# Kernel optimization log

Hardware: AMD Instinct MI355X
Metric: run time of the kernel (lower is better)

The kernel has to match this reference:

```python
import jax, jax.numpy as jnp
import numpy as np

NI = 50000      # input nodes
NO = 50000      # output nodes
DEG = 16        # uniform neighborhood size -> E = NO*DEG
E = NO * DEG
FI = 64         # input feature dim
UNITS = 64
D = 3           # coord feature dim


def setup_inputs() -> dict:
    key = jax.random.key(0)
    k1, k2, k3, k4 = jax.random.split(key, 4)
    node_features = jax.random.normal(k1, (NI, FI), dtype=jnp.float32)
    coord_features = jax.random.normal(k2, (E, D), dtype=jnp.float32)
    indices = jax.random.randint(k3, (E,), 0, NI, dtype=jnp.int64)
    # uniform ragged structure: each output node has DEG edges
    row_splits = (jnp.arange(NO + 1, dtype=jnp.int64) * DEG)
    W = jax.random.normal(k4, (FI, UNITS * D), dtype=jnp.float32) * (1.0 / np.sqrt(FI))
    b = jnp.zeros((UNITS * D,), dtype=jnp.float32)
    return {"node_features": node_features, "coord_features": coord_features,
            "indices": indices, "row_splits": row_splits, "W": W, "b": b}


def reference(node_features, coord_features, indices, row_splits, W, b):
    # Dense projection on input nodes: [Ni, units*D]
    h = node_features @ W + b
    # gather_first=False path of ragged_convolution_transpose: gather after dense
    g = h[indices]                       # [E, units*D]
    g = g.reshape(-1, UNITS, D)          # [E, units, D]
    # contract over coord dim: f_eu = sum_d g_eud * coord_ed
    f = jnp.einsum('eud,ed->eu', g, coord_features)  # [E, units]
    # activation is None (identity)
    # ragged segment-sum via row_splits -> segment ids per edge
    num_out = row_splits.shape[0] - 1
    row_lengths = jnp.diff(row_splits)
    seg_ids = jnp.repeat(jnp.arange(num_out), row_lengths,
                         total_repeat_length=f.shape[0])
    out = jax.ops.segment_sum(f, seg_ids, num_segments=num_out)  # [No, units]
    return out
```

## Files before the change

### kernel.cpp

```cpp
#include <hip/hip_runtime.h>


#define NI 50000
#define NO 50000
#define DEG 16
#define FI 64
#define UNITS 64
#define KK 192
#define TN 16
#define SG 196
#define NBLK 1024
#define NTILES (NO / TN)

__global__ __launch_bounds__(256, 4)
void rct_fused2(const float* __restrict__ nf,
                const float* __restrict__ coord,
                const int* __restrict__ idx,
                const float* __restrict__ W,
                const float* __restrict__ b,
                float* __restrict__ out) {
    __shared__ float G[TN * SG];
    __shared__ float Pbuf[4][TN][UNITS];
    __shared__ float Cs[2][TN][4];
    __shared__ float bs[KK];

    const int tid  = threadIdx.x;
    const int w    = tid >> 6;
    const int lane = tid & 63;

    if (tid < KK) bs[tid] = b[tid];

    float wreg[48];
    #pragma unroll
    for (int j = 0; j < 48; ++j) {
        const int il = j / 3, d = j - il * 3;
        wreg[j] = W[(w * 16 + il) * KK + 3 * lane + d];
    }

    for (int t = blockIdx.x; t < NTILES; t += NBLK) {
        const int node0 = t * TN;
        const int par = t & 1;

        #pragma unroll
        for (int r = 0; r < 4; ++r) {
            const int n  = w * 4 + r;
            const int eb = (node0 + n) * DEG;
            float a0 = 0.f, a1 = 0.f, a2 = 0.f;
            float c0s = 0.f, c1s = 0.f, c2s = 0.f;
            #pragma unroll
            for (int j = 0; j < DEG; ++j) {
                const int e  = __builtin_amdgcn_readfirstlane(eb + j);
                const int id = __builtin_amdgcn_readfirstlane(idx[e]);
                const float c0 = coord[e * 3 + 0];
                const float c1 = coord[e * 3 + 1];
                const float c2 = coord[e * 3 + 2];
                const float v  = nf[id * FI + lane];
                a0 += v * c0; a1 += v * c1; a2 += v * c2;
                c0s += c0; c1s += c1; c2s += c2;
            }
            G[n * SG + 3 * lane + 0] = a0;
            G[n * SG + 3 * lane + 1] = a1;
            G[n * SG + 3 * lane + 2] = a2;
            if (lane == 0) {
                Cs[par][n][0] = c0s; Cs[par][n][1] = c1s; Cs[par][n][2] = c2s;
            }
        }
        __syncthreads();

        {
            float acc[TN];
            #pragma unroll
            for (int n = 0; n < TN; ++n) acc[n] = 0.f;
            const int kbase = w * 48;
            #pragma unroll
            for (int n = 0; n < TN; ++n) {
                const float* g = &G[n * SG + kbase];
                #pragma unroll
                for (int kk = 0; kk < 48; kk += 4) {
                    const float4 gv = *(const float4*)(g + kk);
                    acc[n] += gv.x * wreg[kk]     + gv.y * wreg[kk + 1]
                            + gv.z * wreg[kk + 2] + gv.w * wreg[kk + 3];
                }
            }
            #pragma unroll
            for (int n = 0; n < TN; ++n) Pbuf[w][n][lane] = acc[n];
        }
        __syncthreads();

        #pragma unroll
        for (int jj = 0; jj < 4; ++jj) {
            const int n = w + 4 * jj;
            const float s = Pbuf[0][n][lane] + Pbuf[1][n][lane]
                          + Pbuf[2][n][lane] + Pbuf[3][n][lane]
                          + Cs[par][n][0] * bs[3 * lane + 0]
                          + Cs[par][n][1] * bs[3 * lane + 1]
                          + Cs[par][n][2] * bs[3 * lane + 2];
            out[(node0 + n) * UNITS + lane] = s;
        }
    }
}

extern "C" void kernel_launch(void* const* d_in, const int* in_sizes, int n_in,
                              void* d_out, int out_size, void* d_ws, size_t ws_size,
                              hipStream_t stream) {
    const float* nf    = (const float*)d_in[0];
    const float* coord = (const float*)d_in[1];
    const int*   idx   = (const int*)d_in[2];
    const float* W     = (const float*)d_in[4];
    const float* b     = (const float*)d_in[5];
    float* out = (float*)d_out;

    rct_fused2<<<dim3(NBLK), dim3(256), 0, stream>>>(nf, coord, idx, W, b, out);
}
```

Before: 122.0 us.

## Replace scalar FP32 projection with split-bf16 MFMA and double-buffered LDS

The per-tile 16x192x64 projection now runs on MFMA 16x16x32 bf16 instructions instead of scalar FMAs with a cross-wave reduction. Each operand is split into high and low bf16 parts and three MFMAs are issued per step to approximate FP32 accuracy. The staged G tile is double-buffered, which removes the Pbuf reduction and the second barrier. The cost is extra bit-splitting work and some precision loss compared with true FP32. The gather phase is likely memory-bound, so the gain may be limited.

```diff
diff --git a/kernel.cpp b/kernel.cpp
--- a/kernel.cpp
+++ b/kernel.cpp
@@ -1,101 +1,105 @@
 #include <hip/hip_runtime.h>
 
 
-#define NI 50000
 #define NO 50000
 #define DEG 16
 #define FI 64
 #define UNITS 64
 #define KK 192
 #define TN 16
-#define SG 196
+#define NSTEP 6
+#define GPAD 200
 #define NBLK 1024
 #define NTILES (NO / TN)
 
+typedef __attribute__((ext_vector_type(8))) short short8;
+typedef __attribute__((ext_vector_type(4))) float float4v;
+
+static __device__ __forceinline__ unsigned int asu(float x){ union{float f;unsigned int u;}c; c.f=x; return c.u; }
+static __device__ __forceinline__ float asf(unsigned int x){ union{unsigned int u;float f;}c; c.u=x; return c.f; }
+
 __global__ __launch_bounds__(256, 4)
-void rct_fused2(const float* __restrict__ nf,
-                const float* __restrict__ coord,
-                const int* __restrict__ idx,
-                const float* __restrict__ W,
-                const float* __restrict__ b,
-                float* __restrict__ out) {
-    __shared__ float G[TN * SG];
-    __shared__ float Pbuf[4][TN][UNITS];
+void rct3(const float* __restrict__ nf, const float* __restrict__ coord,
+          const int* __restrict__ idx, const float* __restrict__ W,
+          const float* __restrict__ b, float* __restrict__ out)
+{
+    __shared__ __align__(16) unsigned short Ghi[2][TN][GPAD];
+    __shared__ __align__(16) unsigned short Glo[2][TN][GPAD];
     __shared__ float Cs[2][TN][4];
-    __shared__ float bs[KK];
 
     const int tid  = threadIdx.x;
     const int w    = tid >> 6;
     const int lane = tid & 63;
+    const int m16  = lane & 15;
+    const int quad = lane >> 4;
 
-    if (tid < KK) bs[tid] = b[tid];
+    const int u = 16 * w + m16;
+    short8 Bhi[NSTEP], Blo[NSTEP];
+    #pragma unroll
+    for (int s = 0; s < NSTEP; ++s) {
+        #pragma unroll
+        for (int j = 0; j < 8; ++j) {
+            const int k = s * 32 + quad * 8 + j;
+            const int i = k / 3, d = k - 3 * i;
+            const float v = W[i * KK + 3 * u + d];
+            const unsigned int vb = asu(v);
+            const unsigned int rh = (vb + 0x7FFFu + ((vb >> 16) & 1u)) >> 16;
+            const float hf = asf(rh << 16);
+            Bhi[s][j] = (short)rh;
+            Blo[s][j] = (short)(asu(v - hf) >> 16);
+        }
+    }
+    const float b0 = b[3*u+0], b1 = b[3*u+1], b2 = b[3*u+2];
 
-    float wreg[48];
-    #pragma unroll
-    for (int j = 0; j < 48; ++j) {
-        const int il = j / 3, d = j - il * 3;
-        wreg[j] = W[(w * 16 + il) * KK + 3 * lane + d];
-    }
-
-    for (int t = blockIdx.x; t < NTILES; t += NBLK) {
+    int pp = 0;
+    for (int t = blockIdx.x; t < NTILES; t += NBLK, pp ^= 1) {
         const int node0 = t * TN;
-        const int par = t & 1;
 
         #pragma unroll
         for (int r = 0; r < 4; ++r) {
-            const int n  = w * 4 + r;
+            const int n  = 4 * w + r;
             const int eb = (node0 + n) * DEG;
-            float a0 = 0.f, a1 = 0.f, a2 = 0.f;
-            float c0s = 0.f, c1s = 0.f, c2s = 0.f;
+            float a0=0.f,a1=0.f,a2=0.f,c0s=0.f,c1s=0.f,c2s=0.f;
             #pragma unroll
             for (int j = 0; j < DEG; ++j) {
                 const int e  = __builtin_amdgcn_readfirstlane(eb + j);
                 const int id = __builtin_amdgcn_readfirstlane(idx[e]);
-                const float c0 = coord[e * 3 + 0];
-                const float c1 = coord[e * 3 + 1];
-                const float c2 = coord[e * 3 + 2];
+                const float c0 = coord[3*e+0];
+                const float c1 = coord[3*e+1];
+                const float c2 = coord[3*e+2];
                 const float v  = nf[id * FI + lane];
-                a0 += v * c0; a1 += v * c1; a2 += v * c2;
+                a0 += v*c0; a1 += v*c1; a2 += v*c2;
                 c0s += c0; c1s += c1; c2s += c2;
             }
-            G[n * SG + 3 * lane + 0] = a0;
-            G[n * SG + 3 * lane + 1] = a1;
-            G[n * SG + 3 * lane + 2] = a2;
+            const unsigned int x0=asu(a0), x1=asu(a1), x2=asu(a2);
+            Ghi[pp][n][3*lane+0] = (unsigned short)(x0>>16);
+            Ghi[pp][n][3*lane+1] = (unsigned short)(x1>>16);
+            Ghi[pp][n][3*lane+2] = (unsigned short)(x2>>16);
+            Glo[pp][n][3*lane+0] = (unsigned short)(asu(a0 - asf(x0 & 0xFFFF0000u))>>16);
+            Glo[pp][n][3*lane+1] = (unsigned short)(asu(a1 - asf(x1 & 0xFFFF0000u))>>16);
+            Glo[pp][n][3*lane+2] = (unsigned short)(asu(a2 - asf(x2 & 0xFFFF0000u))>>16);
             if (lane == 0) {
-                Cs[par][n][0] = c0s; Cs[par][n][1] = c1s; Cs[par][n][2] = c2s;
+                Cs[pp][n][0]=c0s; Cs[pp][n][1]=c1s; Cs[pp][n][2]=c2s; Cs[pp][n][3]=0.f;
             }
         }
         __syncthreads();
 
-        {
-            float acc[TN];
-            #pragma unroll
-            for (int n = 0; n < TN; ++n) acc[n] = 0.f;
-            const int kbase = w * 48;
-            #pragma unroll
-            for (int n = 0; n < TN; ++n) {
-                const float* g = &G[n * SG + kbase];
-                #pragma unroll
-                for (int kk = 0; kk < 48; kk += 4) {
-                    const float4 gv = *(const float4*)(g + kk);
-                    acc[n] += gv.x * wreg[kk]     + gv.y * wreg[kk + 1]
-                            + gv.z * wreg[kk + 2] + gv.w * wreg[kk + 3];
-                }
-            }
-            #pragma unroll
-            for (int n = 0; n < TN; ++n) Pbuf[w][n][lane] = acc[n];
+        float4v acc = {0.f, 0.f, 0.f, 0.f};
+        #pragma unroll
+        for (int s = 0; s < NSTEP; ++s) {
+            const short8 Ahi = *(const short8*)(&Ghi[pp][m16][s*32 + quad*8]);
+            const short8 Alo = *(const short8*)(&Glo[pp][m16][s*32 + quad*8]);
+            acc = __builtin_amdgcn_mfma_f32_16x16x32_bf16(Ahi, Bhi[s], acc, 0, 0, 0);
+            acc = __builtin_amdgcn_mfma_f32_16x16x32_bf16(Ahi, Blo[s], acc, 0, 0, 0);
+            acc = __builtin_amdgcn_mfma_f32_16x16x32_bf16(Alo, Bhi[s], acc, 0, 0, 0);
         }
-        __syncthreads();
 
         #pragma unroll
-        for (int jj = 0; jj < 4; ++jj) {
-            const int n = w + 4 * jj;
-            const float s = Pbuf[0][n][lane] + Pbuf[1][n][lane]
-                          + Pbuf[2][n][lane] + Pbuf[3][n][lane]
-                          + Cs[par][n][0] * bs[3 * lane + 0]
-                          + Cs[par][n][1] * bs[3 * lane + 1]
-                          + Cs[par][n][2] * bs[3 * lane + 2];
-            out[(node0 + n) * UNITS + lane] = s;
+        for (int reg = 0; reg < 4; ++reg) {
+            const int row = quad * 4 + reg;
+            const float4v c = *(const float4v*)(&Cs[pp][row][0]);
+            out[(node0 + row) * UNITS + u] =
+                acc[reg] + c[0]*b0 + c[1]*b1 + c[2]*b2;
         }
     }
 }
@@ -110,5 +114,5 @@
     const float* b     = (const float*)d_in[5];
     float* out = (float*)d_out;
 
-    rct_fused2<<<dim3(NBLK), dim3(256), 0, stream>>>(nf, coord, idx, W, b, out);
+    rct3<<<dim3(NBLK), dim3(256), 0, stream>>>(nf, coord, idx, W, b, out);
 }
```

Result: faster. 110.0 us (-9.9%).
